# Kernel optimization log

Hardware: AMD Instinct MI355X
Metric: run time of the kernel (lower is better)

The kernel has to match this reference:

```python
import jax, jax.numpy as jnp
import numpy as np

MAX_PERIOD = 10000.0


def _rope(x, ts):
    # x: [B,H,T,D], ts: [B,T] integer positions (per-batch offset + arange(T))
    B, H, T, D = x.shape
    half = D // 2
    freqs = jnp.exp(jnp.arange(half, dtype=jnp.float32) * (-np.log(MAX_PERIOD) * 2.0 / D))
    ang = ts.astype(jnp.float32)[:, None, :, None] * freqs  # [B,1,T,half]
    cos, sin = jnp.cos(ang), jnp.sin(ang)
    xr = x.reshape(B, H, T, half, 2)  # interleaved (real, imag) pairs
    r, i = xr[..., 0], xr[..., 1]
    out = jnp.stack([r * cos - i * sin, r * sin + i * cos], axis=-1)
    return out.reshape(B, H, T, D)


def setup_inputs() -> dict:
    key = jax.random.key(0)
    ks = jax.random.split(key, 7)
    B, T, C = 8, 128, 1024
    H, D, CAP = 16, 64, 2048
    return {
        'x': jax.random.normal(ks[0], (B, T, C), dtype=jnp.float32),
        'w_in': jax.random.normal(ks[1], (3 * C, C), dtype=jnp.float32) * 0.02,
        'w_out': jax.random.normal(ks[2], (C, C), dtype=jnp.float32) * 0.02,
        'cache_k': jax.random.normal(ks[3], (B, H, CAP, D), dtype=jnp.float32),
        'cache_v': jax.random.normal(ks[4], (B, H, CAP, D), dtype=jnp.float32),
        'end_offset': jax.random.randint(ks[5], (B,), 0, CAP).astype(jnp.int64) if jax.config.jax_enable_x64 else jax.random.randint(ks[5], (B,), 0, CAP),
        'exec_mask': jnp.ones((B,), dtype=bool),
    }


def reference(x, w_in, w_out, cache_k, cache_v, end_offset, exec_mask):
    B, T, C = x.shape
    H, CAP = cache_k.shape[1], cache_k.shape[2]
    D = C // H
    context = CAP  # capacity == self.context

    # fused in-projection, split per rearrange 'b t (p h d) -> p b h t d', p=3
    qkv = (x @ w_in.T).reshape(B, T, 3, H, D).transpose(2, 0, 3, 1, 4)
    q, k, v = qkv[0], qkv[1], qkv[2]  # each [B,H,T,D]

    ts = end_offset[:, None] + jnp.arange(T)  # [B,T] absolute positions of new tokens
    q = _rope(q, ts)
    k = _rope(k, ts)

    # ring-buffer scatter (RingKVCache.complete)
    idx = ts % CAP  # [B,T]
    bI = jnp.arange(B)[:, None, None]
    hI = jnp.arange(H)[None, :, None]
    cache_k = cache_k.at[bI, hI, idx[:, None, :]].set(k)
    cache_v = cache_v.at[bI, hI, idx[:, None, :]].set(v)

    # absolute position of every cache slot, -1 for invalid slots
    cap_idx = jnp.arange(CAP)
    last = end_offset + T - 1  # [B]
    end_index = last % CAP
    delta = cap_idx[None, :] - end_index[:, None]  # [B,CAP]
    positions = jnp.where(delta <= 0, last[:, None] + delta, last[:, None] + delta - CAP)
    new_end = jnp.where(exec_mask, end_offset + T, end_offset)
    positions = jnp.where(cap_idx[None, :] >= new_end[:, None], -1, positions)

    # causal + context mask derived from positions
    d = ts[:, :, None] - positions[:, None, :]  # [B,T,CAP]
    mask = (positions[:, None, :] >= 0) & (d >= 0) & (d < context)

    scale = 1.0 / np.sqrt(D)
    scores = jnp.einsum('bhtd,bhsd->bhts', q, cache_k) * scale  # [B,H,T,CAP]
    scores = jnp.where(mask[:, None], scores, jnp.asarray(-1e9, scores.dtype))
    attn = jax.nn.softmax(scores, axis=-1)
    out = jnp.einsum('bhts,bhsd->bhtd', attn, cache_v)
    out = out.transpose(0, 2, 1, 3).reshape(B, T, C)  # 'b h t d -> b t (h d)'
    return out @ w_out.T
```

## Files before the change

### kernel.cpp

```cpp
#include <hip/hip_runtime.h>
#include <math.h>

#define BB 8
#define TT 128
#define CC 1024
#define HH 16
#define DD 64
#define CAP 2048

typedef __attribute__((ext_vector_type(8))) short short8;
typedef __attribute__((ext_vector_type(4))) short short4v;
typedef __attribute__((ext_vector_type(4))) float float4v;
typedef _Float16 half8 __attribute__((ext_vector_type(8)));
typedef _Float16 half4v __attribute__((ext_vector_type(4)));

__device__ __forceinline__ short f2bf(float x) {
    union { float f; unsigned u; } un; un.f = x;
    unsigned r = (un.u + 0x7FFF + ((un.u >> 16) & 1)) >> 16;
    return (short)r;
}
__device__ __forceinline__ unsigned cvt_pk_bf16(float a, float b) {
    unsigned r;
    asm("v_cvt_pk_bf16_f32 %0, %1, %2" : "=v"(r) : "v"(a), "v"(b));
    return r;
}

__global__ __launch_bounds__(256) void split_all(const float* __restrict__ x,
                                                 const float* __restrict__ w_in,
                                                 const float* __restrict__ w_out,
                                                 _Float16* __restrict__ xhi,
                                                 _Float16* __restrict__ xlo,
                                                 _Float16* __restrict__ wh,
                                                 _Float16* __restrict__ woh) {
    size_t i = ((size_t)blockIdx.x * 256 + threadIdx.x) * 4;
    if (i < (size_t)1048576) {
        float4 f = *(const float4*)(x + i);
        half4v h, l;
        h.x = (_Float16)f.x; l.x = (_Float16)(f.x - (float)h.x);
        h.y = (_Float16)f.y; l.y = (_Float16)(f.y - (float)h.y);
        h.z = (_Float16)f.z; l.z = (_Float16)(f.z - (float)h.z);
        h.w = (_Float16)f.w; l.w = (_Float16)(f.w - (float)h.w);
        *(half4v*)(xhi + i) = h;
        *(half4v*)(xlo + i) = l;
    } else if (i < (size_t)4194304) {
        size_t off = i - 1048576;
        float4 f = *(const float4*)(w_in + off);
        half4v h;
        h.x = (_Float16)f.x; h.y = (_Float16)f.y; h.z = (_Float16)f.z; h.w = (_Float16)f.w;
        *(half4v*)(wh + off) = h;
    } else {
        size_t off = i - 4194304;
        float4 f = *(const float4*)(w_out + off);
        half4v h;
        h.x = (_Float16)f.x; h.y = (_Float16)f.y; h.z = (_Float16)f.z; h.w = (_Float16)f.w;
        *(half4v*)(woh + off) = h;
    }
}

template <int ROWS>
__device__ __forceinline__ void stage_glds(const unsigned short* __restrict__ src,
                                           unsigned short* lds, int K, int wv, int lane) {
#pragma unroll
    for (int c = wv; c < ROWS / 16; c += 4) {
        int row = c * 16 + (lane >> 2);
        int g = lane & 3;
        const unsigned short* ga = src + (size_t)row * K + g * 8;
        unsigned short* la = lds + c * 512 + lane * 8;
        __builtin_amdgcn_global_load_lds((__attribute__((address_space(1))) const unsigned short*)ga,
                                         (__attribute__((address_space(3))) unsigned short*)la,
                                         16, 0, 0);
    }
}

template <int MT, int NT>
__global__ __launch_bounds__(256) void gemm_f16x2(const _Float16* __restrict__ Ahi,
                                                  const _Float16* __restrict__ Alo,
                                                  const _Float16* __restrict__ Bh,
                                                  float* __restrict__ C, int M, int N, int K) {
    constexpr int BM = 2 * MT * 16, BN = 2 * NT * 16;
    __shared__ __align__(16) _Float16 As_h[BM * 32];
    __shared__ __align__(16) _Float16 As_l[BM * 32];
    __shared__ __align__(16) _Float16 Bs[BN * 32];

    int tid = threadIdx.x;
    int lane = tid & 63, wv = tid >> 6;
    int wr = wv >> 1, wc = wv & 1;
    int quad = lane >> 4, lq = lane & 15;
    int m0 = blockIdx.y * BM, n0 = blockIdx.x * BN;

    float4v acc[MT][NT];
#pragma unroll
    for (int mt = 0; mt < MT; ++mt)
#pragma unroll
        for (int nt = 0; nt < NT; ++nt) acc[mt][nt] = (float4v){0.f, 0.f, 0.f, 0.f};

    const unsigned short* a_h = (const unsigned short*)(Ahi + (size_t)m0 * K);
    const unsigned short* a_l = (const unsigned short*)(Alo + (size_t)m0 * K);
    const unsigned short* b_h = (const unsigned short*)(Bh + (size_t)n0 * K);

    for (int k0 = 0; k0 < K; k0 += 32) {
        __syncthreads();
        stage_glds<BM>(a_h + k0, (unsigned short*)As_h, K, wv, lane);
        stage_glds<BM>(a_l + k0, (unsigned short*)As_l, K, wv, lane);
        stage_glds<BN>(b_h + k0, (unsigned short*)Bs, K, wv, lane);
        __syncthreads();

        half8 ah[MT], al[MT];
#pragma unroll
        for (int mt = 0; mt < MT; ++mt) {
            int row = wr * MT * 16 + mt * 16 + lq;
            ah[mt] = *(const half8*)&As_h[row * 32 + quad * 8];
            al[mt] = *(const half8*)&As_l[row * 32 + quad * 8];
        }
#pragma unroll
        for (int nt = 0; nt < NT; ++nt) {
            int row = wc * NT * 16 + nt * 16 + lq;
            half8 bh = *(const half8*)&Bs[row * 32 + quad * 8];
#pragma unroll
            for (int mt = 0; mt < MT; ++mt) {
                float4v c = acc[mt][nt];
                c = __builtin_amdgcn_mfma_f32_16x16x32_f16(ah[mt], bh, c, 0, 0, 0);
                c = __builtin_amdgcn_mfma_f32_16x16x32_f16(al[mt], bh, c, 0, 0, 0);
                acc[mt][nt] = c;
            }
        }
    }

#pragma unroll
    for (int mt = 0; mt < MT; ++mt)
#pragma unroll
        for (int nt = 0; nt < NT; ++nt) {
            int n = n0 + wc * NT * 16 + nt * 16 + lq;
#pragma unroll
            for (int r = 0; r < 4; ++r) {
                int m = m0 + wr * MT * 16 + mt * 16 + quad * 4 + r;
                C[(size_t)m * N + n] = acc[mt][nt][r];
            }
        }
}

__global__ __launch_bounds__(256) void rope_scatter(const float* __restrict__ qkv,
                                                    unsigned short* __restrict__ q_bf,
                                                    float* __restrict__ cache_k,
                                                    float* __restrict__ cache_v,
                                                    const int* __restrict__ end_offset) {
    int gid = blockIdx.x * 256 + threadIdx.x;
    int j = gid & 31;
    int h = (gid >> 5) & 15;
    int t = (gid >> 9) & 127;
    int b = gid >> 16;

    int ts = end_offset[b] + t;
    int slot = ts & (CAP - 1);

    float freq = expf(-0.28782313662425574f * (float)j);
    float ang = (float)ts * freq;
    float s, c;
    sincosf(ang, &s, &c);

    const float* base = qkv + (size_t)(b * TT + t) * (3 * CC);
    int col = h * DD + 2 * j;
    float2 qv = *(const float2*)&base[col];
    float2 kv = *(const float2*)&base[CC + col];
    float2 vv = *(const float2*)&base[2 * CC + col];

    float qr = qv.x * c - qv.y * s;
    float qi = qv.x * s + qv.y * c;
    float kr = kv.x * c - kv.y * s;
    float ki = kv.x * s + kv.y * c;

    size_t qo = ((size_t)(b * HH + h) * TT + t) * DD + 2 * j;
    ushort2 qp;
    qp.x = (unsigned short)f2bf(qr * 0.125f);
    qp.y = (unsigned short)f2bf(qi * 0.125f);
    *(ushort2*)&q_bf[qo] = qp;
    size_t ko = ((size_t)(b * HH + h) * CAP + slot) * DD + 2 * j;
    *(float2*)&cache_k[ko] = make_float2(kr, ki);
    *(float2*)&cache_v[ko] = vv;
}

template <int TPB, bool FBK>
__global__ __launch_bounds__(256) void attn_mfma(const unsigned short* __restrict__ qb,
                                                 const float* __restrict__ ck,
                                                 const float* __restrict__ cv,
                                                 const int* __restrict__ endo,
                                                 const unsigned char* __restrict__ emb,
                                                 const int* __restrict__ emi,
                                                 float* __restrict__ pacc_a,
                                                 float* __restrict__ pacc_b,
                                                 float* __restrict__ pml) {
    __shared__ __align__(16) short k_s[64 * 72];
    __shared__ __align__(16) short v_t[64 * 64];
    __shared__ __align__(16) short p_s[4][16 * 72];

    int tid = threadIdx.x;
    int lane = tid & 63, wv = tid >> 6;
    int quad = lane >> 4, lq = lane & 15;

    int f = blockIdx.x;
    int b = -1, rem = 0, ntiles = 0;
    int cum = 0;
#pragma unroll
    for (int bb = 0; bb < 8; ++bb) {
        int e0 = endo[bb];
        int emx = (emb[bb] != 0) || (emi[bb] != 0);
        int ne = emx ? (e0 + TT) : e0;
        int seb = ne < CAP ? ne : CAP;
        int ntb = (seb + 63) >> 6;
        int nsb = (ntb + TPB - 1) / TPB;
        int wbl = 32 * nsb;
        if (b < 0 && f < cum + wbl) { b = bb; rem = f - cum; ntiles = ntb; }
        cum += wbl;
    }
    if (b < 0) return;
    int sid = rem >> 5;
    int hq = rem & 31;
    int h = hq & 15, qc2 = hq >> 4;
    int tstart = sid * TPB;
    int tend = tstart + TPB < ntiles ? tstart + TPB : ntiles;

    int qrow = qc2 * 64 + wv * 16 + lq;
    int end0 = endo[b];
    int em = (emb[b] != 0) || (emi[b] != 0);
    int last = end0 + TT - 1;
    int end_index = last & (CAP - 1);
    int new_end = em ? (end0 + TT) : end0;
    int se = new_end < CAP ? new_end : CAP;

    int tq = end0 + qrow;
    int tq0 = end0 + qc2 * 64 + wv * 16;
    int len_bad = last - tq0;
    int a_bad = (tq0 + 1) & (CAP - 1);

    const unsigned short* qrp = qb + ((size_t)(b * HH + h) * TT + qrow) * DD;
    short8 aq0 = *(const short8*)(qrp + quad * 8);
    short8 aq1 = *(const short8*)(qrp + 32 + quad * 8);

    const float* kg = ck + (size_t)(b * HH + h) * CAP * DD;
    const float* vg = cv + (size_t)(b * HH + h) * CAP * DD;

    int k_row = tid >> 4, k_f4 = tid & 15;
    float4 kreg[4];
    float vreg[2][8];

    auto ldK = [&](int sb) {
#pragma unroll
        for (int i = 0; i < 4; ++i)
            kreg[i] = *(const float4*)&kg[(size_t)(sb + k_row + 16 * i) * DD + k_f4 * 4];
    };
    auto ldV = [&](int sb) {
#pragma unroll
        for (int gi = 0; gi < 2; ++gi) {
            int g = wv + gi * 4;
#pragma unroll
            for (int i = 0; i < 8; ++i)
                vreg[gi][i] = vg[(size_t)(sb + g * 8 + i) * DD + lane];
        }
    };

    float m = 0.f, l = 0.f;
    float4v acc[4];
#pragma unroll
    for (int mt = 0; mt < 4; ++mt) acc[mt] = (float4v){0.f, 0.f, 0.f, 0.f};

    ldK(tstart * 64);
    ldV(tstart * 64);

    for (int t = tstart; t < tend; ++t) {
        int s0 = t * 64;
        __syncthreads();
#pragma unroll
        for (int i = 0; i < 4; ++i) {
            float4 fv = kreg[i];
            uint2 u;
            u.x = cvt_pk_bf16(fv.x, fv.y);
            u.y = cvt_pk_bf16(fv.z, fv.w);
            *(uint2*)&k_s[(k_row + 16 * i) * 72 + k_f4 * 4] = u;
        }
#pragma unroll
        for (int gi = 0; gi < 2; ++gi) {
            int g = wv + gi * 4;
            uint4 u;
            u.x = cvt_pk_bf16(vreg[gi][0], vreg[gi][1]);
            u.y = cvt_pk_bf16(vreg[gi][2], vreg[gi][3]);
            u.z = cvt_pk_bf16(vreg[gi][4], vreg[gi][5]);
            u.w = cvt_pk_bf16(vreg[gi][6], vreg[gi][7]);
            *(uint4*)&v_t[lane * 64 + (g ^ (lane & 7)) * 8] = u;
        }
        __syncthreads();
        if (t + 1 < tend) {
            ldK((t + 1) * 64);
            ldV((t + 1) * 64);
        }

        float4v sc[4];
#pragma unroll
        for (int nt = 0; nt < 4; ++nt) {
            const short* kr = &k_s[(nt * 16 + lq) * 72 + quad * 8];
            short8 bk0 = *(const short8*)kr;
            short8 bk1 = *(const short8*)(kr + 32);
            float4v c = (float4v){0.f, 0.f, 0.f, 0.f};
            c = __builtin_amdgcn_mfma_f32_16x16x32_bf16(bk0, aq0, c, 0, 0, 0);
            c = __builtin_amdgcn_mfma_f32_16x16x32_bf16(bk1, aq1, c, 0, 0, 0);
            sc[nt] = c;
        }

        int off = (s0 - a_bad) & (CAP - 1);
        bool fast = (off >= len_bad) && (off <= CAP - 64) && (s0 + 63 < se);
        float x[4][4];
        if (fast) {
#pragma unroll
            for (int nt = 0; nt < 4; ++nt)
#pragma unroll
                for (int r = 0; r < 4; ++r) x[nt][r] = sc[nt][r];
        } else {
#pragma unroll
            for (int nt = 0; nt < 4; ++nt)
#pragma unroll
                for (int r = 0; r < 4; ++r) {
                    int s = s0 + nt * 16 + quad * 4 + r;
                    int delta = s - end_index;
                    int pos = (delta <= 0) ? (last + delta) : (last + delta - CAP);
                    bool valid = (s < se) && (pos <= tq);
                    x[nt][r] = valid ? sc[nt][r] : -1.0e30f;
                }
        }

        float v01 = fmaxf(fmaxf(x[0][0], x[0][1]), fmaxf(x[0][2], x[0][3]));
        float v23 = fmaxf(fmaxf(x[1][0], x[1][1]), fmaxf(x[1][2], x[1][3]));
        float v45 = fmaxf(fmaxf(x[2][0], x[2][1]), fmaxf(x[2][2], x[2][3]));
        float v67 = fmaxf(fmaxf(x[3][0], x[3][1]), fmaxf(x[3][2], x[3][3]));
        float vm = fmaxf(fmaxf(v01, v23), fmaxf(v45, v67));
        vm = fmaxf(vm, __shfl_xor(vm, 16, 64));
        vm = fmaxf(vm, __shfl_xor(vm, 32, 64));
        float mn = fmaxf(m, vm);
        float al = __expf(m - mn);
        float ps = 0.f;
#pragma unroll
        for (int nt = 0; nt < 4; ++nt)
#pragma unroll
            for (int r = 0; r < 4; ++r) {
                float p = __expf(x[nt][r] - mn);
                x[nt][r] = p;
                ps += p;
            }
        ps += __shfl_xor(ps, 16, 64);
        ps += __shfl_xor(ps, 32, 64);
        l = l * al + ps;
        m = mn;

#pragma unroll
        for (int nt = 0; nt < 4; ++nt) {
            uint2 u;
            u.x = cvt_pk_bf16(x[nt][0], x[nt][1]);
            u.y = cvt_pk_bf16(x[nt][2], x[nt][3]);
            *(uint2*)&p_s[wv][lq * 72 + nt * 16 + quad * 4] = u;
        }

        short8 bp0 = *(const short8*)&p_s[wv][lq * 72 + quad * 8];
        short8 bp1 = *(const short8*)&p_s[wv][lq * 72 + 32 + quad * 8];
#pragma unroll
        for (int mt = 0; mt < 4; ++mt) {
            int d = mt * 16 + lq;
            const short* vr = &v_t[d * 64];
            short8 av0 = *(const short8*)(vr + ((quad ^ (d & 7)) * 8));
            short8 av1 = *(const short8*)(vr + (((4 + quad) ^ (d & 7)) * 8));
            float4v a = acc[mt];
            a.x *= al; a.y *= al; a.z *= al; a.w *= al;
            a = __builtin_amdgcn_mfma_f32_16x16x32_bf16(av0, bp0, a, 0, 0, 0);
            a = __builtin_amdgcn_mfma_f32_16x16x32_bf16(av1, bp1, a, 0, 0, 0);
            acc[mt] = a;
        }
    }

    int base_row = (b * HH + h) * TT + qc2 * 64;
    float* pa;
    if constexpr (FBK)
        pa = (sid < 3) ? (pacc_a + (size_t)sid * (16384 * 64)) : pacc_b;
    else
        pa = pacc_a + (size_t)sid * (16384 * 64);
    int row_g = base_row + wv * 16 + lq;
#pragma unroll
    for (int mt = 0; mt < 4; ++mt)
        *(float4v*)&pa[(size_t)row_g * 64 + mt * 16 + quad * 4] = acc[mt];
    if (quad == 0) {
        size_t ix = ((size_t)sid * 16384 + row_g) * 2;
        pml[ix] = m;
        pml[ix + 1] = l;
    }
}

template <int TPB, bool FBK>
__global__ __launch_bounds__(256) void attn_combine(const float* __restrict__ pacc_a,
                                                    const float* __restrict__ pacc_b,
                                                    const float* __restrict__ pml,
                                                    const int* __restrict__ endo,
                                                    const unsigned char* __restrict__ emb,
                                                    const int* __restrict__ emi,
                                                    _Float16* __restrict__ ahi,
                                                    _Float16* __restrict__ alo) {
    constexpr int MAXS = FBK ? 4 : 8;
    int gid = blockIdx.x * 256 + threadIdx.x;
    int row = gid >> 6, d = gid & 63;
    int b = row >> 11;

    int e0 = endo[b];
    int emx = (emb[b] != 0) || (emi[b] != 0);
    int ne = emx ? (e0 + TT) : e0;
    int seb = ne < CAP ? ne : CAP;
    int ntb = (seb + 63) >> 6;
    int ns = (ntb + TPB - 1) / TPB;

    float mv[MAXS], lv[MAXS];
#pragma unroll
    for (int s = 0; s < MAXS; ++s) {
        mv[s] = 0.f; lv[s] = 0.f;
        if (s < ns) {
            size_t ix = ((size_t)s * 16384 + row) * 2;
            mv[s] = pml[ix];
            lv[s] = pml[ix + 1];
        }
    }
    float M = 0.f;
#pragma unroll
    for (int s = 0; s < MAXS; ++s) M = fmaxf(M, mv[s]);
    float O = 0.f, L = 0.f;
#pragma unroll
    for (int s = 0; s < MAXS; ++s) {
        if (s < ns && lv[s] > 0.f) {
            const float* pa;
            if constexpr (FBK)
                pa = (s < 3) ? (pacc_a + (size_t)s * (16384 * 64)) : pacc_b;
            else
                pa = pacc_a + (size_t)s * (16384 * 64);
            float w = __expf(mv[s] - M);
            L += w * lv[s];
            O += w * pa[(size_t)row * 64 + d];
        }
    }
    float o = (L > 0.f) ? (O / L) : 0.f;

    int bq = row >> 11, h = (row >> 7) & 15, q = row & 127;
    size_t ob = ((size_t)(bq * TT + q)) * CC + h * DD + d;
    _Float16 hi = (_Float16)o;
    ahi[ob] = hi;
    alo[ob] = (_Float16)(o - (float)hi);
}

extern "C" void kernel_launch(void* const* d_in, const int* in_sizes, int n_in,
                              void* d_out, int out_size, void* d_ws, size_t ws_size,
                              hipStream_t stream) {
    const float* x = (const float*)d_in[0];
    const float* w_in = (const float*)d_in[1];
    const float* w_out = (const float*)d_in[2];
    float* cache_k = (float*)d_in[3];
    float* cache_v = (float*)d_in[4];
    const int* end_offset = (const int*)d_in[5];
    const unsigned char* exec_mask_b = (const unsigned char*)d_in[6];
    const int* exec_mask_i = (const int*)d_in[6];
    float* out = (float*)d_out;

    const size_t MB = 1024 * 1024;
    char* w = (char*)d_ws;
    float* qkv = (float*)w;
    unsigned short* q_bf = (unsigned short*)(w + 12 * MB);
    _Float16* xhi = (_Float16*)(w + 14 * MB);
    _Float16* xlo = (_Float16*)(w + 16 * MB);
    _Float16* wh  = (_Float16*)(w + 18 * MB);
    _Float16* woh = (_Float16*)(w + 24 * MB);
    _Float16* ahi = (_Float16*)(w + 26 * MB);
    _Float16* alo = (_Float16*)(w + 28 * MB);

    bool big = ws_size >= 72 * MB;

    split_all<<<5120, 256, 0, stream>>>(x, w_in, w_out, xhi, xlo, wh, woh);
    gemm_f16x2<2, 4><<<dim3(3072 / 128, 1024 / 64), 256, 0, stream>>>(
        xhi, xlo, wh, qkv, BB * TT, 3 * CC, CC);
    rope_scatter<<<(BB * TT * HH * 32) / 256, 256, 0, stream>>>(
        qkv, q_bf, cache_k, cache_v, end_offset);

    if (big) {
        float* pacc = (float*)(w + 38 * MB);
        float* pml  = (float*)(w + 70 * MB);
        attn_mfma<4, false><<<2048, 256, 0, stream>>>(
            q_bf, cache_k, cache_v, end_offset, exec_mask_b, exec_mask_i,
            pacc, nullptr, pml);
        attn_combine<4, false><<<(16384 * 64) / 256, 256, 0, stream>>>(
            pacc, nullptr, pml, end_offset, exec_mask_b, exec_mask_i, ahi, alo);
    } else {
        float* pacc012 = qkv;
        float* pacc3 = (float*)xhi;
        float* pml = (float*)wh;
        attn_mfma<8, true><<<1024, 256, 0, stream>>>(
            q_bf, cache_k, cache_v, end_offset, exec_mask_b, exec_mask_i,
            pacc012, pacc3, pml);
        attn_combine<8, true><<<(16384 * 64) / 256, 256, 0, stream>>>(
            pacc012, pacc3, pml, end_offset, exec_mask_b, exec_mask_i, ahi, alo);
    }

    gemm_f16x2<2, 2><<<dim3(1024 / 64, 1024 / 64), 256, 0, stream>>>(
        ahi, alo, woh, out, BB * TT, CC, CC);
}
```

Measured before the change: 232.8 us.

## Add cache preheat kernel, vectorize combine, retile QKV GEMM, hoist K/V loads

```diff
diff --git a/kernel.cpp b/kernel.cpp
--- a/kernel.cpp
+++ b/kernel.cpp
@@ -179,6 +179,62 @@
     *(float2*)&cache_v[ko] = vv;
 }
 
+__global__ __launch_bounds__(256) void preheat(const float* __restrict__ ck,
+                                               const float* __restrict__ cv,
+                                               const int* __restrict__ endo,
+                                               const unsigned char* __restrict__ emb,
+                                               const int* __restrict__ emi) {
+    int nt[8];
+    int cumu[9];
+    cumu[0] = 0;
+#pragma unroll
+    for (int bb = 0; bb < 8; ++bb) {
+        int e0 = endo[bb];
+        int emx = (emb[bb] != 0) || (emi[bb] != 0);
+        int ne = emx ? (e0 + TT) : e0;
+        int seb = ne < CAP ? ne : CAP;
+        int ntb = (seb + 63) >> 6;
+        nt[bb] = ntb * 64;
+        cumu[bb + 1] = cumu[bb] + HH * ntb * 64 * 16;
+    }
+    int total = cumu[8];
+    const float4* ck4 = (const float4*)ck;
+    const float4* cv4 = (const float4*)cv;
+    int stride = gridDim.x * 256;
+    float accx = 0.f, accy = 0.f, accz = 0.f, accw = 0.f;
+    for (int u0 = blockIdx.x * 256 + threadIdx.x; u0 < total; u0 += stride * 8) {
+        float4 av[8], bv[8];
+#pragma unroll
+        for (int i = 0; i < 8; ++i) {
+            int u = u0 + i * stride;
+            av[i] = make_float4(0.f, 0.f, 0.f, 0.f);
+            bv[i] = make_float4(0.f, 0.f, 0.f, 0.f);
+            if (u < total) {
+                int b = 0;
+#pragma unroll
+                for (int bb = 1; bb < 8; ++bb)
+                    if (u >= cumu[bb]) b = bb;
+                int off = u - cumu[b];
+                int per_h = nt[b] * 16;
+                int h = off / per_h;
+                int rem = off - h * per_h;
+                size_t f4 = (size_t)(b * HH + h) * (CAP * 16) + rem;
+                av[i] = ck4[f4];
+                bv[i] = cv4[f4];
+            }
+        }
+#pragma unroll
+        for (int i = 0; i < 8; ++i) {
+            accx += av[i].x + bv[i].x;
+            accy += av[i].y + bv[i].y;
+            accz += av[i].z + bv[i].z;
+            accw += av[i].w + bv[i].w;
+        }
+    }
+    float acc = accx + accy + accz + accw;
+    asm volatile("" :: "v"(acc));
+}
+
 template <int TPB, bool FBK>
 __global__ __launch_bounds__(256) void attn_mfma(const unsigned short* __restrict__ qb,
                                                  const float* __restrict__ ck,
@@ -232,10 +288,6 @@
     int len_bad = last - tq0;
     int a_bad = (tq0 + 1) & (CAP - 1);
 
-    const unsigned short* qrp = qb + ((size_t)(b * HH + h) * TT + qrow) * DD;
-    short8 aq0 = *(const short8*)(qrp + quad * 8);
-    short8 aq1 = *(const short8*)(qrp + 32 + quad * 8);
-
     const float* kg = ck + (size_t)(b * HH + h) * CAP * DD;
     const float* vg = cv + (size_t)(b * HH + h) * CAP * DD;
 
@@ -258,13 +310,17 @@
         }
     };
 
+    ldK(tstart * 64);
+    ldV(tstart * 64);
+
+    const unsigned short* qrp = qb + ((size_t)(b * HH + h) * TT + qrow) * DD;
+    short8 aq0 = *(const short8*)(qrp + quad * 8);
+    short8 aq1 = *(const short8*)(qrp + 32 + quad * 8);
+
     float m = 0.f, l = 0.f;
     float4v acc[4];
 #pragma unroll
     for (int mt = 0; mt < 4; ++mt) acc[mt] = (float4v){0.f, 0.f, 0.f, 0.f};
-
-    ldK(tstart * 64);
-    ldV(tstart * 64);
 
     for (int t = tstart; t < tend; ++t) {
         int s0 = t * 64;
@@ -399,9 +455,9 @@
                                                     const int* __restrict__ emi,
                                                     _Float16* __restrict__ ahi,
                                                     _Float16* __restrict__ alo) {
-    constexpr int MAXS = FBK ? 4 : 8;
+    constexpr int MAXS = FBK ? 4 : (32 / TPB);
     int gid = blockIdx.x * 256 + threadIdx.x;
-    int row = gid >> 6, d = gid & 63;
+    int row = gid >> 4, dq = gid & 15, d = dq * 4;
     int b = row >> 11;
 
     int e0 = endo[b];
@@ -411,40 +467,48 @@
     int ntb = (seb + 63) >> 6;
     int ns = (ntb + TPB - 1) / TPB;
 
-    float mv[MAXS], lv[MAXS];
+    float2 ml[MAXS];
+    float4 pv[MAXS];
 #pragma unroll
     for (int s = 0; s < MAXS; ++s) {
-        mv[s] = 0.f; lv[s] = 0.f;
+        ml[s] = make_float2(0.f, 0.f);
+        pv[s] = make_float4(0.f, 0.f, 0.f, 0.f);
         if (s < ns) {
-            size_t ix = ((size_t)s * 16384 + row) * 2;
-            mv[s] = pml[ix];
-            lv[s] = pml[ix + 1];
-        }
-    }
-    float M = 0.f;
-#pragma unroll
-    for (int s = 0; s < MAXS; ++s) M = fmaxf(M, mv[s]);
-    float O = 0.f, L = 0.f;
-#pragma unroll
-    for (int s = 0; s < MAXS; ++s) {
-        if (s < ns && lv[s] > 0.f) {
+            ml[s] = *(const float2*)&pml[((size_t)s * 16384 + row) * 2];
             const float* pa;
             if constexpr (FBK)
                 pa = (s < 3) ? (pacc_a + (size_t)s * (16384 * 64)) : pacc_b;
             else
                 pa = pacc_a + (size_t)s * (16384 * 64);
-            float w = __expf(mv[s] - M);
-            L += w * lv[s];
-            O += w * pa[(size_t)row * 64 + d];
-        }
-    }
-    float o = (L > 0.f) ? (O / L) : 0.f;
-
-    int bq = row >> 11, h = (row >> 7) & 15, q = row & 127;
-    size_t ob = ((size_t)(bq * TT + q)) * CC + h * DD + d;
-    _Float16 hi = (_Float16)o;
-    ahi[ob] = hi;
-    alo[ob] = (_Float16)(o - (float)hi);
+            pv[s] = *(const float4*)&pa[(size_t)row * 64 + d];
+        }
+    }
+    float M = 0.f;
+#pragma unroll
+    for (int s = 0; s < MAXS; ++s) M = fmaxf(M, ml[s].x);
+    float L = 0.f;
+    float ox = 0.f, oy = 0.f, oz = 0.f, ow = 0.f;
+#pragma unroll
+    for (int s = 0; s < MAXS; ++s) {
+        if (s < ns && ml[s].y > 0.f) {
+            float w = __expf(ml[s].x - M);
+            L += w * ml[s].y;
+            ox += w * pv[s].x; oy += w * pv[s].y;
+            oz += w * pv[s].z; ow += w * pv[s].w;
+        }
+    }
+    float inv = (L > 0.f) ? (1.f / L) : 0.f;
+    ox *= inv; oy *= inv; oz *= inv; ow *= inv;
+
+    int h = (row >> 7) & 15, q = row & 127;
+    size_t ob = ((size_t)(b * TT + q)) * CC + h * DD + d;
+    half4v h4, l4;
+    h4.x = (_Float16)ox; l4.x = (_Float16)(ox - (float)h4.x);
+    h4.y = (_Float16)oy; l4.y = (_Float16)(oy - (float)h4.y);
+    h4.z = (_Float16)oz; l4.z = (_Float16)(oz - (float)h4.z);
+    h4.w = (_Float16)ow; l4.w = (_Float16)(ow - (float)h4.w);
+    *(half4v*)&ahi[ob] = h4;
+    *(half4v*)&alo[ob] = l4;
 }
 
 extern "C" void kernel_launch(void* const* d_in, const int* in_sizes, int n_in,
@@ -471,21 +535,21 @@
     _Float16* ahi = (_Float16*)(w + 26 * MB);
     _Float16* alo = (_Float16*)(w + 28 * MB);
 
-    bool big = ws_size >= 72 * MB;
-
     split_all<<<5120, 256, 0, stream>>>(x, w_in, w_out, xhi, xlo, wh, woh);
-    gemm_f16x2<2, 4><<<dim3(3072 / 128, 1024 / 64), 256, 0, stream>>>(
+    gemm_f16x2<2, 2><<<dim3(3072 / 64, 1024 / 64), 256, 0, stream>>>(
         xhi, xlo, wh, qkv, BB * TT, 3 * CC, CC);
     rope_scatter<<<(BB * TT * HH * 32) / 256, 256, 0, stream>>>(
         qkv, q_bf, cache_k, cache_v, end_offset);
-
-    if (big) {
+    preheat<<<1024, 256, 0, stream>>>(cache_k, cache_v, end_offset,
+                                      exec_mask_b, exec_mask_i);
+
+    if (ws_size >= 72 * MB) {
         float* pacc = (float*)(w + 38 * MB);
         float* pml  = (float*)(w + 70 * MB);
         attn_mfma<4, false><<<2048, 256, 0, stream>>>(
             q_bf, cache_k, cache_v, end_offset, exec_mask_b, exec_mask_i,
             pacc, nullptr, pml);
-        attn_combine<4, false><<<(16384 * 64) / 256, 256, 0, stream>>>(
+        attn_combine<4, false><<<(16384 * 16) / 256, 256, 0, stream>>>(
             pacc, nullptr, pml, end_offset, exec_mask_b, exec_mask_i, ahi, alo);
     } else {
         float* pacc012 = qkv;
@@ -494,7 +558,7 @@
         attn_mfma<8, true><<<1024, 256, 0, stream>>>(
             q_bf, cache_k, cache_v, end_offset, exec_mask_b, exec_mask_i,
             pacc012, pacc3, pml);
-        attn_combine<8, true><<<(16384 * 64) / 256, 256, 0, stream>>>(
+        attn_combine<8, true><<<(16384 * 16) / 256, 256, 0, stream>>>(
             pacc012, pacc3, pml, end_offset, exec_mask_b, exec_mask_i, ahi, alo);
     }
 
```

Measured after the change: 242.3 us. 1.04x slower.
